# Performance work log

Measured on AMD Instinct MI355X. Metric: run time of the kernel, lower is better.

The kernel has to match this reference:

```python
import jax, jax.numpy as jnp
import numpy as np

H, W = 1024, 1024
NUM_FEATURES = 64
NUM_PILLARS = 100000


def setup_inputs() -> dict:
    key = jax.random.key(0)
    k1, k2 = jax.random.split(key)
    pillar_features = jax.random.normal(k1, (NUM_PILLARS, NUM_FEATURES), dtype=jnp.float32)
    coords = jax.random.randint(k2, (NUM_PILLARS, 3), 0, 1024, dtype=jnp.int64)
    return {"pillar_features": pillar_features, "coords": coords}


def reference(pillar_features, coords):
    # pillar_features: [N, F]; coords: [N, 3] = (batch_idx, y_idx, x_idx)
    x_idx = coords[:, 2]
    y_idx = coords[:, 1]
    valid = (x_idx >= 0) & (x_idx < W) & (y_idx >= 0) & (y_idx < H)
    # Flatten spatial dims; route invalid pillars to an out-of-bounds slot
    # that mode='drop' discards (matches the torch valid_mask filtering).
    flat_idx = jnp.where(valid, y_idx * W + x_idx, H * W)
    img = jnp.zeros((NUM_FEATURES, H * W), dtype=pillar_features.dtype)
    # single vectorized scatter: [F, N] updates into [F, H*W]
    img = img.at[:, flat_idx].set(pillar_features.T, mode='drop')
    return img.reshape(1, NUM_FEATURES, H, W)
```

## Files before the change

kernel.cpp:

```cpp
#include <hip/hip_runtime.h>


constexpr int H    = 1024;
constexpr int W    = 1024;
constexpr int HW   = H * W;
constexpr int NF   = 64;
constexpr int TILE = 256;
constexpr int HALF = 32;

typedef float nt4 __attribute__((ext_vector_type(4)));

__global__ void winner_kernel(const int* __restrict__ coords,
                              int* __restrict__ winner, int np) {
    int p = blockIdx.x * blockDim.x + threadIdx.x;
    if (p >= np) return;
    int y = coords[p * 3 + 1];
    int x = coords[p * 3 + 2];
    if ((unsigned)x < (unsigned)W && (unsigned)y < (unsigned)H) {
        atomicMax(winner + (y * W + x), p);
    }
}

__global__ void __launch_bounds__(256) fill_kernel(const float* __restrict__ feat,
                                                   const int* __restrict__ winner,
                                                   float* __restrict__ out) {
    __shared__ float lds[HALF * TILE];

    const int base = blockIdx.x * TILE;
    const int t    = threadIdx.x;
    const int wp   = winner[base + t];
    const int wv   = t >> 6;
    const int l    = t & 63;

    const float4* row = (const float4*)(feat + (size_t)max(wp, 0) * NF);

#pragma unroll
    for (int h = 0; h < 2; ++h) {
        if (wp >= 0) {
#pragma unroll
            for (int j = 0; j < 8; ++j) {
                float4 r = row[h * 8 + j];
                lds[(j * 4 + 0) * TILE + t] = r.x;
                lds[(j * 4 + 1) * TILE + t] = r.y;
                lds[(j * 4 + 2) * TILE + t] = r.z;
                lds[(j * 4 + 3) * TILE + t] = r.w;
            }
        } else {
#pragma unroll
            for (int j = 0; j < HALF; ++j) lds[j * TILE + t] = 0.0f;
        }
        __syncthreads();

#pragma unroll
        for (int p = 0; p < 8; ++p) {
            const int floc = p * 4 + wv;
            nt4 v = *(const nt4*)&lds[floc * TILE + l * 4];
            __builtin_nontemporal_store(
                v, (nt4*)(out + (size_t)(h * HALF + floc) * HW + base + l * 4));
        }
        __syncthreads();
    }
}

extern "C" void kernel_launch(void* const* d_in, const int* in_sizes, int n_in,
                              void* d_out, int out_size, void* d_ws, size_t ws_size,
                              hipStream_t stream) {
    const float* feat   = (const float*)d_in[0];
    const int*   coords = (const int*)d_in[1];
    float*       out    = (float*)d_out;
    int np = in_sizes[1] / 3;

    int* winner = (int*)d_ws;

    (void)hipMemsetAsync(winner, 0xFF, (size_t)HW * sizeof(int), stream);
    winner_kernel<<<(np + 255) / 256, 256, 0, stream>>>(coords, winner, np);
    fill_kernel<<<HW / TILE, 256, 0, stream>>>(feat, winner, out);
}
```

Measured before the change: 297.9 us.

## Cooperative coalesced gather of pillar rows with XOR-swizzled LDS transpose

Rather than each thread reading its own pillar's 128-byte half-row as eight float4 loads, eight threads now share one pillar, each loading one float4, so a row segment comes in as a single coalesced access. Winner indices are first staged in shared memory, and LDS columns are XOR-swizzled, with the matching unswizzle on readback, to avoid bank conflicts in the transposed writes. The cost is an extra barrier plus index arithmetic per element.

After: 318.3 us. +6.8%, slower.

```diff
diff --git a/kernel.cpp b/kernel.cpp
--- a/kernel.cpp
+++ b/kernel.cpp
@@ -25,36 +25,46 @@
                                                    const int* __restrict__ winner,
                                                    float* __restrict__ out) {
     __shared__ float lds[HALF * TILE];
+    __shared__ int   wc[TILE];
 
     const int base = blockIdx.x * TILE;
     const int t    = threadIdx.x;
-    const int wp   = winner[base + t];
     const int wv   = t >> 6;
     const int l    = t & 63;
+    const int q    = t & 7;
+    const int g    = t >> 3;
+    const int xorX = (q & 3) << 3;
 
-    const float4* row = (const float4*)(feat + (size_t)max(wp, 0) * NF);
+    wc[t] = winner[base + t];
+    __syncthreads();
 
+    for (int h = 0; h < 2; ++h) {
 #pragma unroll
-    for (int h = 0; h < 2; ++h) {
-        if (wp >= 0) {
-#pragma unroll
-            for (int j = 0; j < 8; ++j) {
-                float4 r = row[h * 8 + j];
-                lds[(j * 4 + 0) * TILE + t] = r.x;
-                lds[(j * 4 + 1) * TILE + t] = r.y;
-                lds[(j * 4 + 2) * TILE + t] = r.z;
-                lds[(j * 4 + 3) * TILE + t] = r.w;
+        for (int r = 0; r < 8; ++r) {
+            const int c   = r * 32 + g;
+            const int wp  = wc[c];
+            const int col = c ^ xorX;
+            float* dst = lds + (q * 4) * TILE + col;
+            if (wp >= 0) {
+                float4 v = *(const float4*)(feat + (size_t)wp * NF + h * HALF + q * 4);
+                dst[0 * TILE] = v.x;
+                dst[1 * TILE] = v.y;
+                dst[2 * TILE] = v.z;
+                dst[3 * TILE] = v.w;
+            } else {
+                dst[0 * TILE] = 0.0f;
+                dst[1 * TILE] = 0.0f;
+                dst[2 * TILE] = 0.0f;
+                dst[3 * TILE] = 0.0f;
             }
-        } else {
-#pragma unroll
-            for (int j = 0; j < HALF; ++j) lds[j * TILE + t] = 0.0f;
         }
         __syncthreads();
 
 #pragma unroll
         for (int p = 0; p < 8; ++p) {
             const int floc = p * 4 + wv;
-            nt4 v = *(const nt4*)&lds[floc * TILE + l * 4];
+            const int X    = (p & 3) << 3;
+            nt4 v = *(const nt4*)&lds[floc * TILE + ((l * 4) ^ X)];
             __builtin_nontemporal_store(
                 v, (nt4*)(out + (size_t)(h * HALF + floc) * HW + base + l * 4));
         }
```
